# Kernel tuning notes

Hardware: AMD Instinct MI355X
Metric: run time of the kernel (lower is better)

Reference implementation:

```python
import jax, jax.numpy as jnp
import numpy as np

NEG_INF = -9e15  # matches torch's -9000000000000000.0 mask fill
LEAKY_SLOPE = 0.01  # F.leaky_relu default


def setup_inputs() -> dict:
    key = jax.random.key(0)
    ks = jax.random.split(key, 6)
    B, N, F_in, F_out = 4, 4096, 256, 128
    h = jax.random.normal(ks[0], (B, N, F_in), dtype=jnp.float32)
    adj = jax.random.randint(ks[1], (B, N, N), 0, 2, dtype=jnp.int32)
    W_w = jax.random.normal(ks[2], (F_out, F_in), dtype=jnp.float32) * (1.0 / np.sqrt(F_in))
    W_b = jax.random.normal(ks[3], (F_out,), dtype=jnp.float32) * 0.01
    a_w = jax.random.normal(ks[4], (2 * F_out,), dtype=jnp.float32) * (1.0 / np.sqrt(2 * F_out))
    a_b = jax.random.normal(ks[5], (), dtype=jnp.float32) * 0.01
    return {"h": h, "adj": adj, "W_w": W_w, "W_b": W_b, "a_w": a_w, "a_b": a_b}


def reference(h, adj, W_w, W_b, a_w, a_b):
    # Wh: [B, N, F_out]
    Wh = jnp.einsum('bnf,of->bno', h, W_w) + W_b
    F_out = Wh.shape[-1]
    # a([Wh_i, Wh_j]) decomposes as a_src.Wh_i + a_dst.Wh_j + a_b (linearity),
    # avoiding the O(N^2 * 2F) repeat+cat intermediate while computing identical math.
    a_src, a_dst = a_w[:F_out], a_w[F_out:]
    src = jnp.einsum('bno,o->bn', Wh, a_src)  # [B, N]
    dst = jnp.einsum('bno,o->bn', Wh, a_dst)  # [B, N]
    e = src[:, :, None] + dst[:, None, :] + a_b  # [B, N, N]
    e = jnp.where(e >= 0, e, LEAKY_SLOPE * e)  # leaky_relu
    masked = jnp.where(adj > 0, e, NEG_INF)
    attention = jax.nn.softmax(masked, axis=-1)  # row softmax over neighbors j
    h_prime = jnp.einsum('bij,bjo->bio', attention, Wh)
    return h_prime
```

## Files before the change

### kernel.cpp

```cpp
#include <hip/hip_runtime.h>
#include <hip/hip_bf16.h>

typedef __attribute__((ext_vector_type(4))) float f32x4;
typedef __attribute__((ext_vector_type(8))) short s16x8;
typedef unsigned long long u64;

#define NB_ 4
#define N_ 4096
#define FI_ 256
#define FO_ 128
#define NROWS 16384
#define SPLIT 4
#define NSTEPS ((N_ / SPLIT) / 32)

__device__ __forceinline__ unsigned pkbf(float a, float b) {
    __hip_bfloat162 t = __float22bfloat162_rn(make_float2(a, b));
    unsigned r; __builtin_memcpy(&r, &t, 4); return r;
}

typedef __attribute__((address_space(1))) const void CGV;
typedef __attribute__((address_space(3))) void LDSV;
__device__ __forceinline__ void gload16(const void* g, void* l) {
    __builtin_amdgcn_global_load_lds((CGV*)g, (LDSV*)l, 16, 0, 0);
}

__device__ __forceinline__ unsigned encf(float x) {
    unsigned u = __float_as_uint(x);
    return (u & 0x80000000u) ? ~u : (u | 0x80000000u);
}
__device__ __forceinline__ float decf(unsigned v) {
    unsigned u = (v & 0x80000000u) ? (v ^ 0x80000000u) : ~v;
    return __uint_as_float(u);
}

__global__ __launch_bounds__(256) void k0_packw(
    const float* __restrict__ Ww, __hip_bfloat16* __restrict__ whi,
    __hip_bfloat16* __restrict__ wlo)
{
    int idx = blockIdx.x * 256 + threadIdx.x;
    float v = Ww[idx];
    __hip_bfloat16 hi = __float2bfloat16(v);
    whi[idx] = hi;
    wlo[idx] = __float2bfloat16(v - __bfloat162float(hi));
}

__global__ __launch_bounds__(256) void k1_wh(
    const float* __restrict__ h, const __hip_bfloat16* __restrict__ whi,
    const __hip_bfloat16* __restrict__ wlo, const float* __restrict__ Wb,
    const float* __restrict__ aw, const float* __restrict__ ab,
    short* __restrict__ WhTf, float* __restrict__ srcv,
    unsigned* __restrict__ auxp, unsigned* __restrict__ maxenc)
{
    __shared__ float lds[16][132];
    __shared__ float dbsh[16];
    const int tid = threadIdx.x;
    const int w = tid >> 6, l = tid & 63;
    const int lr = l & 15, g = l >> 4;
    const int r0 = blockIdx.x * 16;
    const float* hp = h + (size_t)(r0 + lr) * FI_ + g * 8;

    f32x4 acc[2] = {(f32x4)0.f, (f32x4)0.f};

    #pragma unroll
    for (int kt = 0; kt < 8; ++kt) {
        f32x4 x0 = *(const f32x4*)(hp + kt * 32);
        f32x4 x1 = *(const f32x4*)(hp + kt * 32 + 4);
        float xx[8];
        #pragma unroll
        for (int t = 0; t < 4; ++t) { xx[t] = x0[t]; xx[t + 4] = x1[t]; }
        union { s16x8 v; unsigned u[4]; } ahi, alo;
        #pragma unroll
        for (int t = 0; t < 4; ++t) {
            float a0 = xx[2 * t], a1 = xx[2 * t + 1];
            unsigned uh = pkbf(a0, a1);
            ahi.u[t] = uh;
            float h0f = __uint_as_float(uh << 16);
            float h1f = __uint_as_float(uh & 0xffff0000u);
            alo.u[t] = pkbf(a0 - h0f, a1 - h1f);
        }
        #pragma unroll
        for (int c = 0; c < 2; ++c) {
            const int o = w * 32 + c * 16 + lr;
            s16x8 bh = *(const s16x8*)(whi + (size_t)o * FI_ + kt * 32 + g * 8);
            s16x8 bl = *(const s16x8*)(wlo + (size_t)o * FI_ + kt * 32 + g * 8);
            acc[c] = __builtin_amdgcn_mfma_f32_16x16x32_bf16(ahi.v, bh, acc[c], 0, 0, 0);
            acc[c] = __builtin_amdgcn_mfma_f32_16x16x32_bf16(alo.v, bh, acc[c], 0, 0, 0);
            acc[c] = __builtin_amdgcn_mfma_f32_16x16x32_bf16(ahi.v, bl, acc[c], 0, 0, 0);
        }
    }

    #pragma unroll
    for (int c = 0; c < 2; ++c) {
        int col = w * 32 + c * 16 + lr;
        float wb = Wb[col];
        #pragma unroll
        for (int kk = 0; kk < 4; ++kk)
            lds[g * 4 + kk][col] = acc[c][kk] + wb;
    }
    __syncthreads();

    {
        const int o = tid >> 1, joct = tid & 1;
        const int jblk = (r0 & 4095) >> 5;
        const int bb = r0 >> 12;
        const int lb = ((r0 >> 3) & 3) + joct;
        union { s16x8 v; unsigned u[4]; } af;
        #pragma unroll
        for (int q = 0; q < 4; ++q)
            af.u[q] = pkbf(lds[joct * 8 + 2 * q][o], lds[joct * 8 + 2 * q + 1][o]);
        short* dst = WhTf + (((size_t)bb * 128 + jblk) * 8 + (o >> 4)) * 512
                          + ((o & 15) + 16 * lb) * 8;
        *(s16x8*)dst = af.v;
    }

    {
        const int row = tid >> 4, seg = tid & 15;
        float sp = 0.f, dp = 0.f;
        #pragma unroll
        for (int i = 0; i < 8; ++i) {
            float v = lds[row][seg * 8 + i];
            sp += v * aw[seg * 8 + i];
            dp += v * aw[FO_ + seg * 8 + i];
        }
        #pragma unroll
        for (int off = 8; off >= 1; off >>= 1) {
            sp += __shfl_xor(sp, off);
            dp += __shfl_xor(dp, off);
        }
        if (seg == 0) {
            int r = r0 + row;
            srcv[r] = sp;
            float db = dp + ab[0];
            dbsh[row] = db;
            auxp[r] = pkbf(__expf(db), __expf(0.01f * db));
        }
        __syncthreads();
        if (tid == 0) {
            float m = dbsh[0];
            #pragma unroll
            for (int i = 1; i < 16; ++i) m = fmaxf(m, dbsh[i]);
            atomicMax(&maxenc[r0 >> 12], encf(m));
        }
    }
}

__global__ __launch_bounds__(256, 4) void k3_gat(
    const int* __restrict__ adj, const short* __restrict__ WhTf,
    const float* __restrict__ srcv, const unsigned* __restrict__ auxp,
    const unsigned* __restrict__ maxenc, float* __restrict__ pacc,
    float* __restrict__ prow)
{
    __shared__ int adjb[3][32][32];
    __shared__ __hip_bfloat16 whb[2][4096];
    __shared__ unsigned auxb[2][32];

    const int t = threadIdx.x;
    const int w = t >> 6, l = t & 63;
    const int lr = l & 15, g = l >> 4;
    const int rh = w & 1, oh = w >> 1;
    const int b = blockIdx.x >> 7;
    const int rblk = (blockIdx.x & 127) * 32;
    const int bN = b * N_;
    const int j0 = blockIdx.y * (N_ / SPLIT);

    float C1, C2;
    {
        int r = rblk + rh * 16 + lr;
        float s = srcv[bN + r];
        float eub = s + decf(maxenc[b]);
        float m = fmaxf(eub, 0.01f * eub);
        C1 = __expf(s - m);
        C2 = __expf(0.01f * s - m);
    }

    const unsigned* axsrc = auxp + (size_t)bN + j0;
    const short* whsrc = WhTf + ((size_t)b * 128 + (j0 >> 5)) * 4096;

    f32x4 acc[4];
    #pragma unroll
    for (int ot = 0; ot < 4; ++ot) acc[ot] = (f32x4)0.f;
    float rs = 0.f;

    auto stage_adj = [&](int bi, int s) {
        const int jb = j0 + s * 32;
        const int r = t >> 3, c = t & 7;
        gload16(adj + (size_t)(bN + rblk + r) * N_ + jb + ((c ^ (r & 7)) << 2),
                &adjb[bi][0][0] + w * 256);
    };
    auto stage_wh = [&](int bi, int s) {
        const short* src = whsrc + (size_t)s * 4096;
        #pragma unroll
        for (int i = 0; i < 2; ++i)
            gload16(src + (size_t)(i * 256 + t) * 8,
                    &whb[bi][0] + (size_t)(i * 256 + w * 64) * 8);
    };
    auto stage_aux = [&](int bi, int s) {
        if (l < 2)
            gload16(axsrc + s * 32 + (w * 2 + l) * 4, &auxb[bi][w * 8]);
    };

    stage_adj(0, 0);
    __builtin_amdgcn_sched_barrier(0);
    stage_aux(0, 0);
    stage_wh(0, 0);
    __builtin_amdgcn_sched_barrier(0);
    stage_adj(1, 1);
    __builtin_amdgcn_sched_barrier(0);

    for (int s = 0; s < NSTEPS; ++s) {
        __builtin_amdgcn_sched_barrier(0);
        if (s + 1 < NSTEPS) asm volatile("s_waitcnt vmcnt(1)" ::: "memory");
        else                asm volatile("s_waitcnt vmcnt(0)" ::: "memory");
        __builtin_amdgcn_sched_barrier(0);
        __builtin_amdgcn_s_barrier();
        __builtin_amdgcn_sched_barrier(0);

        const int cur = s & 1, curA = s % 3;
        if (s + 1 < NSTEPS) {
            stage_aux(cur ^ 1, s + 1);
            stage_wh(cur ^ 1, s + 1);
        }
        if (s + 2 < NSTEPS) stage_adj((s + 2) % 3, s + 2);
        __builtin_amdgcn_sched_barrier(0);

        uint4 x0 = *(const uint4*)&auxb[cur][g * 8];
        uint4 x1 = *(const uint4*)&auxb[cur][g * 8 + 4];
        const int R = rh * 16 + lr;
        const int4 a0 = *(const int4*)&adjb[curA][R][((2 * g) ^ (R & 7)) << 2];
        const int4 a1 = *(const int4*)&adjb[curA][R][(((2 * g) + 1) ^ (R & 7)) << 2];
        s16x8 Bf[4];
        #pragma unroll
        for (int ot = 0; ot < 4; ++ot)
            Bf[ot] = *(const s16x8*)&whb[cur][(size_t)((oh * 4 + ot) * 64 + l) * 8];

        const unsigned ax[8] = {x0.x, x0.y, x0.z, x0.w, x1.x, x1.y, x1.z, x1.w};
        const int av[8] = {a0.x, a0.y, a0.z, a0.w, a1.x, a1.y, a1.z, a1.w};
        float p[8];
        #pragma unroll
        for (int e = 0; e < 8; ++e) {
            float e1f = __uint_as_float(ax[e] << 16);
            float e2f = __uint_as_float(ax[e] & 0xffff0000u);
            float v = fmaxf(e1f * C1, e2f * C2);
            p[e] = (av[e] > 0) ? v : 0.f;
            rs += p[e];
        }
        union { s16x8 v; unsigned u[4]; } af;
        af.u[0] = pkbf(p[0], p[1]); af.u[1] = pkbf(p[2], p[3]);
        af.u[2] = pkbf(p[4], p[5]); af.u[3] = pkbf(p[6], p[7]);

        #pragma unroll
        for (int ot = 0; ot < 4; ++ot)
            acc[ot] = __builtin_amdgcn_mfma_f32_16x16x32_bf16(
                af.v, Bf[ot], acc[ot], 0, 0, 0);
    }

    rs += __shfl_xor(rs, 16);
    rs += __shfl_xor(rs, 32);
    if (oh == 0 && g == 0)
        prow[blockIdx.y * NROWS + bN + rblk + rh * 16 + lr] = rs;

    const size_t sb = (size_t)blockIdx.y * ((size_t)NROWS * FO_);
    #pragma unroll
    for (int kk = 0; kk < 4; ++kk) {
        int rloc = rh * 16 + g * 4 + kk;
        int grow = bN + rblk + rloc;
        float* pp = pacc + sb + (size_t)grow * FO_ + oh * 64 + lr;
        #pragma unroll
        for (int ot = 0; ot < 4; ++ot)
            pp[ot * 16] = acc[ot][kk];
    }
}

__global__ __launch_bounds__(256) void k4_comb(
    const float* __restrict__ pacc, const float* __restrict__ prow,
    float* __restrict__ out)
{
    const int idx = blockIdx.x * 256 + threadIdx.x;
    const int grow = idx >> 7;
    float s = 0.f, rs = 0.f;
    #pragma unroll
    for (int si = 0; si < SPLIT; ++si) {
        s  += pacc[(size_t)si * ((size_t)NROWS * FO_) + idx];
        rs += prow[si * NROWS + grow];
    }
    out[idx] = s / rs;
}

extern "C" void kernel_launch(void* const* d_in, const int* in_sizes, int n_in,
                              void* d_out, int out_size, void* d_ws, size_t ws_size,
                              hipStream_t stream)
{
    const float* h  = (const float*)d_in[0];
    const int* adj  = (const int*)d_in[1];
    const float* Ww = (const float*)d_in[2];
    const float* Wb = (const float*)d_in[3];
    const float* aw = (const float*)d_in[4];
    const float* ab = (const float*)d_in[5];
    float* out = (float*)d_out;

    char* wsb = (char*)d_ws;
    float* pacc          = (float*)wsb;
    short* WhTf          = (short*)(wsb + 33554432u);
    char* aux            = wsb + 37748736u;
    float* srcv          = (float*)(aux);
    unsigned* auxp       = (unsigned*)(aux + (64u << 10));
    __hip_bfloat16* whi  = (__hip_bfloat16*)(aux + (128u << 10));
    __hip_bfloat16* wlo  = (__hip_bfloat16*)(aux + (192u << 10));
    unsigned* maxenc     = (unsigned*)(aux + (256u << 10));
    float* prow          = (float*)(aux + (320u << 10));

    hipMemsetAsync(maxenc, 0, NB_ * sizeof(unsigned), stream);
    k0_packw<<<128, 256, 0, stream>>>(Ww, whi, wlo);
    k1_wh<<<1024, 256, 0, stream>>>(h, whi, wlo, Wb, aw, ab, WhTf, srcv, auxp, maxenc);
    dim3 g3(NB_ * 128, SPLIT);
    k3_gat<<<g3, 256, 0, stream>>>(adj, WhTf, srcv, auxp, maxenc, pacc, prow);
    k4_comb<<<8192, 256, 0, stream>>>(pacc, prow, out);
}
```

Measured before the change: 146.7 us.

## Halve split-K, simplify k3 pipeline, vectorize combine, fold memset into packw

Reduces the column split in the attention kernel from four to two, which halves the partial-accumulator traffic and the combine work but also halves the grid. The k3 software pipeline moves from a three-deep adjacency ring with explicit vmcnt waits to plain double buffering with __syncthreads, and the aux values are now loaded directly into registers instead of staged through LDS. The combine kernel is vectorized to float4 and uses one reciprocal per row. The separate memset launch is removed by zeroing maxenc inside k0. The shallower pipeline and the smaller grid of 1024 blocks on 256 CUs may expose more memory latency.

Result: faster. 133.8 us (-8.8%).

```diff
diff --git a/kernel.cpp b/kernel.cpp
--- a/kernel.cpp
+++ b/kernel.cpp
@@ -10,7 +10,7 @@
 #define FI_ 256
 #define FO_ 128
 #define NROWS 16384
-#define SPLIT 4
+#define SPLIT 2
 #define NSTEPS ((N_ / SPLIT) / 32)
 
 __device__ __forceinline__ unsigned pkbf(float a, float b) {
@@ -35,9 +35,10 @@
 
 __global__ __launch_bounds__(256) void k0_packw(
     const float* __restrict__ Ww, __hip_bfloat16* __restrict__ whi,
-    __hip_bfloat16* __restrict__ wlo)
+    __hip_bfloat16* __restrict__ wlo, unsigned* __restrict__ maxenc)
 {
     int idx = blockIdx.x * 256 + threadIdx.x;
+    if (blockIdx.x == 0 && threadIdx.x < NB_) maxenc[threadIdx.x] = 0u;
     float v = Ww[idx];
     __hip_bfloat16 hi = __float2bfloat16(v);
     whi[idx] = hi;
@@ -150,9 +151,9 @@
     const unsigned* __restrict__ maxenc, float* __restrict__ pacc,
     float* __restrict__ prow)
 {
-    __shared__ int adjb[3][32][32];
+    __shared__ int adjb[2][32][32];
     __shared__ __hip_bfloat16 whb[2][4096];
-    __shared__ unsigned auxb[2][32];
+    __shared__ float rsum[32];
 
     const int t = threadIdx.x;
     const int w = t >> 6, l = t & 63;
@@ -173,7 +174,7 @@
         C2 = __expf(0.01f * s - m);
     }
 
-    const unsigned* axsrc = auxp + (size_t)bN + j0;
+    const unsigned* axp = auxp + (size_t)bN + j0 + g * 8;
     const short* whsrc = WhTf + ((size_t)b * 128 + (j0 >> 5)) * 4096;
 
     f32x4 acc[4];
@@ -185,7 +186,7 @@
         const int jb = j0 + s * 32;
         const int r = t >> 3, c = t & 7;
         gload16(adj + (size_t)(bN + rblk + r) * N_ + jb + ((c ^ (r & 7)) << 2),
-                &adjb[bi][0][0] + w * 256);
+                &adjb[bi][0][0] + (size_t)w * 256);
     };
     auto stage_wh = [&](int bi, int s) {
         const short* src = whsrc + (size_t)s * 4096;
@@ -194,47 +195,37 @@
             gload16(src + (size_t)(i * 256 + t) * 8,
                     &whb[bi][0] + (size_t)(i * 256 + w * 64) * 8);
     };
-    auto stage_aux = [&](int bi, int s) {
-        if (l < 2)
-            gload16(axsrc + s * 32 + (w * 2 + l) * 4, &auxb[bi][w * 8]);
-    };
-
+
+    uint4 xc0, xc1;
     stage_adj(0, 0);
-    __builtin_amdgcn_sched_barrier(0);
-    stage_aux(0, 0);
     stage_wh(0, 0);
-    __builtin_amdgcn_sched_barrier(0);
-    stage_adj(1, 1);
-    __builtin_amdgcn_sched_barrier(0);
+    xc0 = *(const uint4*)(axp);
+    xc1 = *(const uint4*)(axp + 4);
+    __syncthreads();
+    int cur = 0;
 
     for (int s = 0; s < NSTEPS; ++s) {
-        __builtin_amdgcn_sched_barrier(0);
-        if (s + 1 < NSTEPS) asm volatile("s_waitcnt vmcnt(1)" ::: "memory");
-        else                asm volatile("s_waitcnt vmcnt(0)" ::: "memory");
-        __builtin_amdgcn_sched_barrier(0);
-        __builtin_amdgcn_s_barrier();
-        __builtin_amdgcn_sched_barrier(0);
-
-        const int cur = s & 1, curA = s % 3;
-        if (s + 1 < NSTEPS) {
-            stage_aux(cur ^ 1, s + 1);
+        uint4 xn0 = {0, 0, 0, 0}, xn1 = {0, 0, 0, 0};
+        const bool more = (s + 1 < NSTEPS);
+        if (more) {
+            stage_adj(cur ^ 1, s + 1);
             stage_wh(cur ^ 1, s + 1);
-        }
-        if (s + 2 < NSTEPS) stage_adj((s + 2) % 3, s + 2);
-        __builtin_amdgcn_sched_barrier(0);
-
-        uint4 x0 = *(const uint4*)&auxb[cur][g * 8];
-        uint4 x1 = *(const uint4*)&auxb[cur][g * 8 + 4];
+            const int jn = (s + 1) * 32;
+            xn0 = *(const uint4*)(axp + jn);
+            xn1 = *(const uint4*)(axp + jn + 4);
+        }
+
+        const unsigned ax[8] = {xc0.x, xc0.y, xc0.z, xc0.w,
+                                xc1.x, xc1.y, xc1.z, xc1.w};
         const int R = rh * 16 + lr;
-        const int4 a0 = *(const int4*)&adjb[curA][R][((2 * g) ^ (R & 7)) << 2];
-        const int4 a1 = *(const int4*)&adjb[curA][R][(((2 * g) + 1) ^ (R & 7)) << 2];
+        const int4 a0 = *(const int4*)&adjb[cur][R][((2 * g) ^ (R & 7)) << 2];
+        const int4 a1 = *(const int4*)&adjb[cur][R][((2 * g + 1) ^ (R & 7)) << 2];
+        const int av[8] = {a0.x, a0.y, a0.z, a0.w, a1.x, a1.y, a1.z, a1.w};
         s16x8 Bf[4];
         #pragma unroll
         for (int ot = 0; ot < 4; ++ot)
             Bf[ot] = *(const s16x8*)&whb[cur][(size_t)((oh * 4 + ot) * 64 + l) * 8];
 
-        const unsigned ax[8] = {x0.x, x0.y, x0.z, x0.w, x1.x, x1.y, x1.z, x1.w};
-        const int av[8] = {a0.x, a0.y, a0.z, a0.w, a1.x, a1.y, a1.z, a1.w};
         float p[8];
         #pragma unroll
         for (int e = 0; e < 8; ++e) {
@@ -252,12 +243,16 @@
         for (int ot = 0; ot < 4; ++ot)
             acc[ot] = __builtin_amdgcn_mfma_f32_16x16x32_bf16(
                 af.v, Bf[ot], acc[ot], 0, 0, 0);
+
+        __syncthreads();
+        xc0 = xn0; xc1 = xn1;
+        cur ^= 1;
     }
 
     rs += __shfl_xor(rs, 16);
     rs += __shfl_xor(rs, 32);
-    if (oh == 0 && g == 0)
-        prow[blockIdx.y * NROWS + bN + rblk + rh * 16 + lr] = rs;
+    if (oh == 0 && g == 0) rsum[rh * 16 + lr] = rs;
+    __syncthreads();
 
     const size_t sb = (size_t)blockIdx.y * ((size_t)NROWS * FO_);
     #pragma unroll
@@ -268,6 +263,8 @@
         #pragma unroll
         for (int ot = 0; ot < 4; ++ot)
             pp[ot * 16] = acc[ot][kk];
+        if (oh == 0 && lr == 0)
+            prow[blockIdx.y * NROWS + grow] = rsum[rloc];
     }
 }
 
@@ -275,15 +272,18 @@
     const float* __restrict__ pacc, const float* __restrict__ prow,
     float* __restrict__ out)
 {
-    const int idx = blockIdx.x * 256 + threadIdx.x;
-    const int grow = idx >> 7;
-    float s = 0.f, rs = 0.f;
+    const int i4 = blockIdx.x * 256 + threadIdx.x;
+    const int grow = i4 >> 5;
+    f32x4 s = (f32x4)0.f;
+    float rs = 0.f;
     #pragma unroll
     for (int si = 0; si < SPLIT; ++si) {
-        s  += pacc[(size_t)si * ((size_t)NROWS * FO_) + idx];
+        s += *(const f32x4*)(pacc + (size_t)si * ((size_t)NROWS * FO_) + (size_t)i4 * 4);
         rs += prow[si * NROWS + grow];
     }
-    out[idx] = s / rs;
+    float inv = 1.0f / rs;
+    f32x4 o = s * inv;
+    *(f32x4*)(out + (size_t)i4 * 4) = o;
 }
 
 extern "C" void kernel_launch(void* const* d_in, const int* in_sizes, int n_in,
@@ -309,10 +309,9 @@
     unsigned* maxenc     = (unsigned*)(aux + (256u << 10));
     float* prow          = (float*)(aux + (320u << 10));
 
-    hipMemsetAsync(maxenc, 0, NB_ * sizeof(unsigned), stream);
-    k0_packw<<<128, 256, 0, stream>>>(Ww, whi, wlo);
+    k0_packw<<<128, 256, 0, stream>>>(Ww, whi, wlo, maxenc);
     k1_wh<<<1024, 256, 0, stream>>>(h, whi, wlo, Wb, aw, ab, WhTf, srcv, auxp, maxenc);
     dim3 g3(NB_ * 128, SPLIT);
     k3_gat<<<g3, 256, 0, stream>>>(adj, WhTf, srcv, auxp, maxenc, pacc, prow);
-    k4_comb<<<8192, 256, 0, stream>>>(pacc, prow, out);
-}
+    k4_comb<<<2048, 256, 0, stream>>>(pacc, prow, out);
+}
```
